# Kernel tuning notes

Hardware: AMD Instinct MI355X
Metric: run time of the kernel (lower is better)

Reference implementation:

```python
import jax, jax.numpy as jnp
import numpy as np

EMBED = 1024
HEADS = 16
HEAD_DIM = EMBED // HEADS


def setup_inputs() -> dict:
    key = jax.random.key(0)
    ks = jax.random.split(key, 9)
    B, S = 2, 2048
    values = jax.random.normal(ks[0], (B, S, EMBED), dtype=jnp.float32)
    keys_in = jax.random.normal(ks[1], (B, S, EMBED), dtype=jnp.float32)
    query = jax.random.normal(ks[2], (B, S, EMBED), dtype=jnp.float32)
    mask = jax.random.randint(ks[3], (B, 1, 1, S), 0, 2, dtype=jnp.int32)
    # torch Linear weights: [out_features, in_features], y = x @ W.T
    sc = 1.0 / np.sqrt(HEAD_DIM)
    Wv = jax.random.uniform(ks[4], (HEAD_DIM, HEAD_DIM), jnp.float32, -sc, sc)
    Wk = jax.random.uniform(ks[5], (HEAD_DIM, HEAD_DIM), jnp.float32, -sc, sc)
    Wq = jax.random.uniform(ks[6], (HEAD_DIM, HEAD_DIM), jnp.float32, -sc, sc)
    so = 1.0 / np.sqrt(EMBED)
    Wo = jax.random.uniform(ks[7], (EMBED, EMBED), jnp.float32, -so, so)
    bo = jax.random.uniform(ks[8], (EMBED,), jnp.float32, -so, so)
    return {"values": values, "keys": keys_in, "query": query, "mask": mask,
            "Wv": Wv, "Wk": Wk, "Wq": Wq, "Wo": Wo, "bo": bo}


def reference(values, keys, query, mask, Wv, Wk, Wq, Wo, bo):
    B = query.shape[0]
    # split heads: [B, S, H, D]
    v = values.reshape(B, -1, HEADS, HEAD_DIM)
    k = keys.reshape(B, -1, HEADS, HEAD_DIM)
    q = query.reshape(B, -1, HEADS, HEAD_DIM)
    # per-head shared linear projections (nn.Linear on last dim, no bias)
    v = jnp.einsum('bshd,ed->bshe', v, Wv)
    k = jnp.einsum('bshd,ed->bshe', k, Wk)
    q = jnp.einsum('bshd,ed->bshe', q, Wq)
    # energy: [B, H, Q, K]
    energy = jnp.einsum('bqhd,bkhd->bhqk', q, k)
    energy = jnp.where(mask == 0, jnp.float32(-1e20), energy)
    attn = jax.nn.softmax(energy / jnp.sqrt(jnp.float32(EMBED)), axis=3)
    out = jnp.einsum('bhqk,bkhd->bqhd', attn, v).reshape(B, -1, EMBED)
    return out @ Wo.T + bo
```

## Files before the change

### kernel.cpp

```cpp
#include <hip/hip_runtime.h>
#include <hip/hip_bf16.h>


typedef __attribute__((ext_vector_type(8))) short bf16x8;
typedef __attribute__((ext_vector_type(4))) float f32x4;
typedef __attribute__((ext_vector_type(16))) float f32x16;
typedef __attribute__((ext_vector_type(2))) int i32x2;

__device__ int g_srcidx[2 * 2048];
__device__ int g_NK[2];

__device__ __forceinline__ short f2bf(float x) {
  union { float f; unsigned u; } v; v.f = x;
  unsigned r = v.u + 0x7FFFu + ((v.u >> 16) & 1u);
  return (short)(r >> 16);
}

__device__ __forceinline__ int pack2(float lo, float hi) {
  __hip_bfloat162 h = __float22bfloat162_rn(make_float2(lo, hi));
  int r; __builtin_memcpy(&r, &h, 4); return r;
}

__device__ __forceinline__ bf16x8 cvt8(float4 a, float4 b) {
  bf16x8 r;
  r[0] = f2bf(a.x); r[1] = f2bf(a.y); r[2] = f2bf(a.z); r[3] = f2bf(a.w);
  r[4] = f2bf(b.x); r[5] = f2bf(b.y); r[6] = f2bf(b.z); r[7] = f2bf(b.w);
  return r;
}

__device__ __forceinline__ void plsw(int& a, int& b) {
  i32x2 r = __builtin_amdgcn_permlane32_swap(a, b, false, false);
  a = r[0]; b = r[1];
}
__device__ __forceinline__ float pl_comb_add(float v) {
  int a = __float_as_int(v), b = a;
  i32x2 r = __builtin_amdgcn_permlane32_swap(a, b, false, false);
  return __int_as_float(r[0]) + __int_as_float(r[1]);
}

__device__ __forceinline__ void gll16(const short* g, short* l) {
  __builtin_amdgcn_global_load_lds(
      (const __attribute__((address_space(1))) void*)g,
      (__attribute__((address_space(3))) void*)l, 16, 0, 0);
}

__global__ __launch_bounds__(256) void prep_kernel(
    const int* __restrict__ mask, const float* __restrict__ Wo,
    short* __restrict__ WoB) {
  __shared__ int cnt[256];
  const int t = threadIdx.x;
  if (blockIdx.x < 2) {
    const int b = blockIdx.x;
    const int* m = mask + b * 2048;
    int* sidx = g_srcidx + b * 2048;
    const int base = t * 8;
    int vals[8], lc = 0;
#pragma unroll
    for (int i = 0; i < 8; i++) { vals[i] = (m[base + i] != 0); lc += vals[i]; }
    cnt[t] = lc;
    __syncthreads();
    for (int off = 1; off < 256; off <<= 1) {
      int v = (t >= off) ? cnt[t - off] : 0;
      __syncthreads();
      cnt[t] += v;
      __syncthreads();
    }
    int pos = cnt[t] - lc;
    const int total = cnt[255];
#pragma unroll
    for (int i = 0; i < 8; i++)
      if (vals[i]) sidx[pos++] = base + i;
    for (int j = total + t; j < 2048; j += 256) sidx[j] = 0;
    if (t == 0) g_NK[b] = total;
  } else {
    int i = ((blockIdx.x - 2) * 256 + t) * 8;
    float4 a = *(const float4*)(Wo + i), b2 = *(const float4*)(Wo + i + 4);
    *(bf16x8*)(WoB + i) = cvt8(a, b2);
  }
}

__global__ __launch_bounds__(256) void proj_kernel(
    const float* __restrict__ keys, const float* __restrict__ query,
    const float* __restrict__ values,
    const float* __restrict__ Wk, const float* __restrict__ Wq,
    const float* __restrict__ Wv,
    short* __restrict__ Kp, short* __restrict__ Qp, short* __restrict__ Vt) {
  const int bid0 = blockIdx.x;
  const int t = threadIdx.x;
  const int w = t >> 6, l = t & 63, l15 = l & 15, l4 = l >> 4;
  __shared__ short Al[64 * 64];
  __shared__ short Bl[64 * 64];
  __shared__ short Tl[64 * 66];

  if (bid0 < 2048) {
    int bid = bid0;
    const float* X = keys; const float* W = Wk; short* O = Kp;
    bool isq = false;
    if (bid >= 1024) { X = query; W = Wq; O = Qp; bid -= 1024; isq = true; }
    const int r0 = bid << 6;
    const int bb = r0 >> 15;
    if (!isq) {
      const int j0 = (r0 >> 4) & 2047;
      const int jlim = (g_NK[bb] + 63) & ~63;
      if (j0 >= jlim) return;
    }
#pragma unroll
    for (int i = 0; i < 2; i++) {
      int c = t + (i << 8);
      int row = c >> 3, col8 = c & 7;
      int pc = col8 ^ (row & 7);
      int ri = r0 + row;
      int j = (ri >> 4) & 2047, hh = ri & 15;
      int s = isq ? j : g_srcidx[(bb << 11) + j];
      const float* xs = X + ((size_t)((bb * 2048 + s) * 16 + hh)) * 64 + col8 * 8;
      float4 a0 = *(const float4*)xs, a1 = *(const float4*)(xs + 4);
      *(bf16x8*)&Al[row * 64 + pc * 8] = cvt8(a0, a1);
      const float* wsrc = W + row * 64 + col8 * 8;
      float4 b0 = *(const float4*)wsrc, b1 = *(const float4*)(wsrc + 4);
      *(bf16x8*)&Bl[row * 64 + pc * 8] = cvt8(b0, b1);
    }
    __syncthreads();
    f32x4 acc[4];
#pragma unroll
    for (int i = 0; i < 4; i++) acc[i] = (f32x4){0.f, 0.f, 0.f, 0.f};
#pragma unroll
    for (int kc = 0; kc < 2; kc++) {
      int ar = w * 16 + l15;
      bf16x8 af = *(const bf16x8*)((const char*)Al +
          ((ar * 128 + kc * 64 + l4 * 16) ^ ((ar & 7) << 4)));
#pragma unroll
      for (int ng = 0; ng < 4; ng++) {
        int br = ng * 16 + l15;
        bf16x8 bfr = *(const bf16x8*)((const char*)Bl +
            ((br * 128 + kc * 64 + l4 * 16) ^ ((br & 7) << 4)));
        acc[ng] = __builtin_amdgcn_mfma_f32_16x16x32_bf16(af, bfr, acc[ng], 0, 0, 0);
      }
    }
    const float osc = isq ? (1.4426950408889634f / 32.0f) : 1.0f;
#pragma unroll
    for (int ng = 0; ng < 4; ng++) {
#pragma unroll
      for (int j = 0; j < 4; j++) {
        int ri = r0 + w * 16 + l4 * 4 + j;
        int e = ng * 16 + l15;
        int b2 = ri >> 15, jj = (ri >> 4) & 2047, hh = ri & 15;
        O[(((size_t)(b2 * 16 + hh)) * 2048 + jj) * 64 + e] = f2bf(acc[ng][j] * osc);
      }
    }
  } else {
    const int bid = bid0 - 2048;
    const int st = bid & 31, bh = bid >> 5;
    const int b = bh >> 4, h = bh & 15;
    const int s0 = st << 6;
    const int jlim = (g_NK[b] + 63) & ~63;
    if (s0 >= jlim) return;
#pragma unroll
    for (int i = 0; i < 2; i++) {
      int c = t + (i << 8);
      int row = c >> 3, col8 = c & 7;
      int pc = col8 ^ (row & 7);
      int s = g_srcidx[(b << 11) + s0 + row];
      const float* xs = values + ((size_t)(b * 2048 + s)) * 1024 + h * 64 + col8 * 8;
      float4 a0 = *(const float4*)xs, a1 = *(const float4*)(xs + 4);
      *(bf16x8*)&Al[row * 64 + pc * 8] = cvt8(a0, a1);
      const float* wsrc = Wv + row * 64 + col8 * 8;
      float4 b0 = *(const float4*)wsrc, b1 = *(const float4*)(wsrc + 4);
      *(bf16x8*)&Bl[row * 64 + pc * 8] = cvt8(b0, b1);
    }
    __syncthreads();
    f32x4 acc[4];
#pragma unroll
    for (int i = 0; i < 4; i++) acc[i] = (f32x4){0.f, 0.f, 0.f, 0.f};
#pragma unroll
    for (int kc = 0; kc < 2; kc++) {
      int ar = w * 16 + l15;
      bf16x8 af = *(const bf16x8*)((const char*)Al +
          ((ar * 128 + kc * 64 + l4 * 16) ^ ((ar & 7) << 4)));
#pragma unroll
      for (int ng = 0; ng < 4; ng++) {
        int br = ng * 16 + l15;
        bf16x8 bfr = *(const bf16x8*)((const char*)Bl +
            ((br * 128 + kc * 64 + l4 * 16) ^ ((br & 7) << 4)));
        acc[ng] = __builtin_amdgcn_mfma_f32_16x16x32_bf16(af, bfr, acc[ng], 0, 0, 0);
      }
    }
#pragma unroll
    for (int ng = 0; ng < 4; ng++) {
#pragma unroll
      for (int j = 0; j < 4; j++) {
        Tl[(w * 16 + l4 * 4 + j) * 66 + ng * 16 + l15] = f2bf(acc[ng][j]);
      }
    }
    __syncthreads();
    int e = t >> 2, sc = (t & 3) << 4;
    bf16x8 o0, o1;
#pragma unroll
    for (int i = 0; i < 8; i++) {
      o0[i] = Tl[(sc + i) * 66 + e];
      o1[i] = Tl[(sc + 8 + i) * 66 + e];
    }
    short* dst = Vt + ((size_t)bh * 64 + e) * 2048 + s0 + sc;
    *(bf16x8*)dst = o0;
    *(bf16x8*)(dst + 8) = o1;
  }
}

__global__ __launch_bounds__(256, 2) void attn_kernel(
    const short* __restrict__ Qp, const short* __restrict__ Kp,
    const short* __restrict__ Vt, short* __restrict__ AO) {
  const int bid = blockIdx.x;
  const int qb = bid & 15, bh = bid >> 4;
  const int b = bh >> 4, h = bh & 15;
  const int t = threadIdx.x;
  const int w = t >> 6, l = t & 63, l31 = l & 31, hi = l >> 5;
  const int q0w = qb * 128 + w * 32;

  __shared__ short Kl[2][64 * 64];
  __shared__ short Vl[2][64 * 64];
  __shared__ float Cl[4 * 32];

  const short* Kbase = Kp + (size_t)bh * 2048 * 64;
  const short* Vbase = Vt + (size_t)bh * 64 * 2048;

  const int nk = g_NK[b];
  const int ntiles = (nk + 63) >> 6;

  const short* qptr = Qp + ((size_t)bh * 2048 + q0w + l31) * 64 + hi * 8;
  bf16x8 qf[4];
#pragma unroll
  for (int dc = 0; dc < 4; dc++) qf[dc] = *(const bf16x8*)(qptr + dc * 16);

  int laddr[2][4];
#pragma unroll
  for (int x = 0; x < 2; x++) {
    int rr = x * 32 + l31;
#pragma unroll
    for (int c2 = 0; c2 < 4; c2++)
      laddr[x][c2] = rr * 128 + (((c2 * 32) + hi * 16) ^ ((rr & 7) << 4));
  }

  const int srow = t >> 3, scol = t & 7;
  const int sc0 = (scol ^ (srow & 7)) * 8;
  const short* ksrc0 = Kbase + srow * 64 + sc0;
  const short* ksrc1 = Kbase + (srow + 32) * 64 + sc0;
  const short* vsrc0 = Vbase + (size_t)srow * 2048 + sc0;
  const short* vsrc1 = Vbase + (size_t)(srow + 32) * 2048 + sc0;
  short* klds = &Kl[0][0];
  short* vlds = &Vl[0][0];
  const int d0 = t * 8, d1 = t * 8 + 2048;

  gll16(ksrc0, klds + d0);
  gll16(ksrc1, klds + d1);
  gll16(vsrc0, vlds + d0);
  gll16(vsrc1, vlds + d1);
  __syncthreads();

  float l_run = 0.f;
  f32x16 o0, o1;
#pragma unroll
  for (int r = 0; r < 16; r++) { o0[r] = 0.f; o1[r] = 0.f; }

  for (int kt = 0; kt < ntiles; kt++) {
    const int bs = kt & 1;
    const int bsb = bs << 13;
    if (kt + 1 < ntiles) {
      const int nb = (bs ^ 1) << 12;
      gll16(ksrc0 + (kt + 1) * 4096, klds + nb + d0);
      gll16(ksrc1 + (kt + 1) * 4096, klds + nb + d1);
      gll16(vsrc0 + (kt + 1) * 64, vlds + nb + d0);
      gll16(vsrc1 + (kt + 1) * 64, vlds + nb + d1);
    }

    f32x16 st0, st1;
#pragma unroll
    for (int r = 0; r < 16; r++) { st0[r] = 0.f; st1[r] = 0.f; }
    __builtin_amdgcn_s_setprio(1);
#pragma unroll
    for (int dc = 0; dc < 4; dc++) {
      bf16x8 ka = *(const bf16x8*)((const char*)Kl + bsb + laddr[0][dc]);
      st0 = __builtin_amdgcn_mfma_f32_32x32x16_bf16(ka, qf[dc], st0, 0, 0, 0);
    }
#pragma unroll
    for (int dc = 0; dc < 4; dc++) {
      bf16x8 kb = *(const bf16x8*)((const char*)Kl + bsb + laddr[1][dc]);
      st1 = __builtin_amdgcn_mfma_f32_32x32x16_bf16(kb, qf[dc], st1, 0, 0, 0);
    }
    __builtin_amdgcn_s_setprio(0);

    if (((kt << 6) + 64) <= nk) {
#pragma unroll
      for (int r = 0; r < 16; r++) {
        st0[r] = __builtin_amdgcn_exp2f(st0[r]);
        st1[r] = __builtin_amdgcn_exp2f(st1[r]);
      }
    } else {
      const int kb2 = kt << 6;
#pragma unroll
      for (int r = 0; r < 16; r++) {
        int cr = (r & 3) + 8 * (r >> 2) + 4 * hi;
        float e0 = __builtin_amdgcn_exp2f(st0[r]);
        float e1 = __builtin_amdgcn_exp2f(st1[r]);
        st0[r] = (kb2 + cr < nk) ? e0 : 0.f;
        st1[r] = (kb2 + 32 + cr < nk) ? e1 : 0.f;
      }
    }

    float sx[8];
#pragma unroll
    for (int i = 0; i < 8; i++)
      sx[i] = (st0[2 * i] + st0[2 * i + 1]) + (st1[2 * i] + st1[2 * i + 1]);
#pragma unroll
    for (int s2 = 4; s2 > 0; s2 >>= 1)
#pragma unroll
      for (int i = 0; i < 4; i++)
        if (i < s2) sx[i] += sx[i + s2];
    l_run += pl_comb_add(sx[0]);

    bf16x8 pa[4];
#pragma unroll
    for (int kc = 0; kc < 4; kc++) {
      int bse = (kc & 1) * 8;
      float p0, p1, p2, p3, p4, p5, p6, p7;
      if (kc < 2) {
        p0 = st0[bse + 0]; p1 = st0[bse + 1]; p2 = st0[bse + 2]; p3 = st0[bse + 3];
        p4 = st0[bse + 4]; p5 = st0[bse + 5]; p6 = st0[bse + 6]; p7 = st0[bse + 7];
      } else {
        p0 = st1[bse + 0]; p1 = st1[bse + 1]; p2 = st1[bse + 2]; p3 = st1[bse + 3];
        p4 = st1[bse + 4]; p5 = st1[bse + 5]; p6 = st1[bse + 6]; p7 = st1[bse + 7];
      }
      int A0 = pack2(p0, p1), A1 = pack2(p2, p3);
      int B0 = pack2(p4, p5), B1 = pack2(p6, p7);
      plsw(A0, B0);
      plsw(A1, B1);
      union { int4 i; bf16x8 h; } u;
      u.i = make_int4(A0, A1, B0, B1);
      pa[kc] = u.h;
    }

    __builtin_amdgcn_s_setprio(1);
#pragma unroll
    for (int kc = 0; kc < 4; kc++) {
      bf16x8 vf = *(const bf16x8*)((const char*)Vl + bsb + laddr[0][kc]);
      o0 = __builtin_amdgcn_mfma_f32_32x32x16_bf16(pa[kc], vf, o0, 0, 0, 0);
    }
#pragma unroll
    for (int kc = 0; kc < 4; kc++) {
      bf16x8 vf = *(const bf16x8*)((const char*)Vl + bsb + laddr[1][kc]);
      o1 = __builtin_amdgcn_mfma_f32_32x32x16_bf16(pa[kc], vf, o1, 0, 0, 0);
    }
    __builtin_amdgcn_s_setprio(0);
    __syncthreads();
  }

  float invr = 1.0f / l_run;
  Cl[w * 32 + l31] = invr;
  short* aob = AO + ((size_t)(b * 2048 + q0w)) * 1024 + h * 64 + l31;
#pragma unroll
  for (int r = 0; r < 16; r++) {
    int qr = (r & 3) + 8 * (r >> 2) + 4 * hi;
    float ic = Cl[w * 32 + qr];
    aob[(size_t)qr * 1024] = f2bf(o0[r] * ic);
    aob[(size_t)qr * 1024 + 32] = f2bf(o1[r] * ic);
  }
}

__global__ __launch_bounds__(256) void outproj_kernel(
    const short* __restrict__ AO, const short* __restrict__ WoB,
    const float* __restrict__ bo, float* __restrict__ Cout) {
  const int bid = blockIdx.x;
  const int mt = bid >> 4, nt = bid & 15;
  const int m0 = mt << 6, n0 = nt << 6;
  const int t = threadIdx.x;
  const int w = t >> 6, l = t & 63, l15 = l & 15, l4 = l >> 4;
  __shared__ short Al[2][64 * 64];
  __shared__ short Bl[2][64 * 64];

  const int srow = t >> 3, scol = t & 7;
  const int sc0 = (scol ^ (srow & 7)) * 8;
  const short* asrc0 = AO + (size_t)(m0 + srow) * 1024 + sc0;
  const short* asrc1 = AO + (size_t)(m0 + srow + 32) * 1024 + sc0;
  const short* bsrc0 = WoB + (size_t)(n0 + srow) * 1024 + sc0;
  const short* bsrc1 = WoB + (size_t)(n0 + srow + 32) * 1024 + sc0;
  short* al = &Al[0][0];
  short* bl = &Bl[0][0];
  const int d0 = t * 8, d1 = t * 8 + 2048;

  gll16(asrc0, al + d0); gll16(asrc1, al + d1);
  gll16(bsrc0, bl + d0); gll16(bsrc1, bl + d1);
  __syncthreads();

  f32x4 acc[4];
#pragma unroll
  for (int i = 0; i < 4; i++) acc[i] = (f32x4){0.f, 0.f, 0.f, 0.f};

  for (int ks = 0; ks < 16; ks++) {
    const int bs = ks & 1, bsb = bs << 13;
    if (ks < 15) {
      const int nb = (bs ^ 1) << 12;
      const int ko = (ks + 1) * 64;
      gll16(asrc0 + ko, al + nb + d0); gll16(asrc1 + ko, al + nb + d1);
      gll16(bsrc0 + ko, bl + nb + d0); gll16(bsrc1 + ko, bl + nb + d1);
    }
#pragma unroll
    for (int kc = 0; kc < 2; kc++) {
      int ar = w * 16 + l15;
      bf16x8 af = *(const bf16x8*)((const char*)Al + bsb +
          ((ar * 128 + kc * 64 + l4 * 16) ^ ((ar & 7) << 4)));
#pragma unroll
      for (int ng = 0; ng < 4; ng++) {
        int br = ng * 16 + l15;
        bf16x8 bfr = *(const bf16x8*)((const char*)Bl + bsb +
            ((br * 128 + kc * 64 + l4 * 16) ^ ((br & 7) << 4)));
        acc[ng] = __builtin_amdgcn_mfma_f32_16x16x32_bf16(af, bfr, acc[ng], 0, 0, 0);
      }
    }
    __syncthreads();
  }
#pragma unroll
  for (int ng = 0; ng < 4; ng++) {
    int n = n0 + ng * 16 + l15;
    float bias = bo[n];
#pragma unroll
    for (int j = 0; j < 4; j++) {
      int m = m0 + w * 16 + l4 * 4 + j;
      Cout[(size_t)m * 1024 + n] = acc[ng][j] + bias;
    }
  }
}

extern "C" void kernel_launch(void* const* d_in, const int* in_sizes, int n_in,
                              void* d_out, int out_size, void* d_ws, size_t ws_size,
                              hipStream_t stream) {
  const float* values = (const float*)d_in[0];
  const float* keys   = (const float*)d_in[1];
  const float* query  = (const float*)d_in[2];
  const int*   mask   = (const int*)d_in[3];
  const float* Wv = (const float*)d_in[4];
  const float* Wk = (const float*)d_in[5];
  const float* Wq = (const float*)d_in[6];
  const float* Wo = (const float*)d_in[7];
  const float* bo = (const float*)d_in[8];
  float* out = (float*)d_out;
  char* ws = (char*)d_ws;
  short* Qp  = (short*)(ws + (size_t)0);
  short* Kp  = (short*)(ws + ((size_t)8 << 20));
  short* Vtp = (short*)(ws + ((size_t)16 << 20));
  short* AO  = (short*)(ws + ((size_t)24 << 20));
  short* WoB = (short*)(ws + ((size_t)32 << 20));

  prep_kernel<<<514, 256, 0, stream>>>(mask, Wo, WoB);
  proj_kernel<<<3072, 256, 0, stream>>>(keys, query, values, Wk, Wq, Wv, Kp, Qp, Vtp);
  attn_kernel<<<512, 256, 0, stream>>>(Qp, Kp, Vtp, AO);
  outproj_kernel<<<1024, 256, 0, stream>>>(AO, WoB, bo, out);
}
```

Before: 70.03 us.

## Process two K/V tiles per barrier with four-buffer LDS pipelining

Restructures the attention main loop so that two 64-key tiles are staged ahead and computed per iteration, with four LDS buffers for K and V. Only one __syncthreads is needed per two tiles, which halves the barrier count, and loads run further ahead of use. It also rewrites cvt8 to use packed bf16 conversions. The cost is doubled LDS use (64KB+ per block), which could lower occupancy below the two blocks per CU the launch bounds request.

After: 70.57 us. Within noise of the previous version (+0.8%).

```diff
diff --git a/kernel.cpp b/kernel.cpp
--- a/kernel.cpp
+++ b/kernel.cpp
@@ -22,10 +22,12 @@
 }
 
 __device__ __forceinline__ bf16x8 cvt8(float4 a, float4 b) {
-  bf16x8 r;
-  r[0] = f2bf(a.x); r[1] = f2bf(a.y); r[2] = f2bf(a.z); r[3] = f2bf(a.w);
-  r[4] = f2bf(b.x); r[5] = f2bf(b.y); r[6] = f2bf(b.z); r[7] = f2bf(b.w);
-  return r;
+  union { int i[4]; bf16x8 h; } u;
+  u.i[0] = pack2(a.x, a.y);
+  u.i[1] = pack2(a.z, a.w);
+  u.i[2] = pack2(b.x, b.y);
+  u.i[3] = pack2(b.z, b.w);
+  return u.h;
 }
 
 __device__ __forceinline__ void plsw(int& a, int& b) {
@@ -215,8 +217,8 @@
   const int w = t >> 6, l = t & 63, l31 = l & 31, hi = l >> 5;
   const int q0w = qb * 128 + w * 32;
 
-  __shared__ short Kl[2][64 * 64];
-  __shared__ short Vl[2][64 * 64];
+  __shared__ short Kl[4][64 * 64];
+  __shared__ short Vl[4][64 * 64];
   __shared__ float Cl[4 * 32];
 
   const short* Kbase = Kp + (size_t)bh * 2048 * 64;
@@ -249,28 +251,21 @@
   short* vlds = &Vl[0][0];
   const int d0 = t * 8, d1 = t * 8 + 2048;
 
-  gll16(ksrc0, klds + d0);
-  gll16(ksrc1, klds + d1);
-  gll16(vsrc0, vlds + d0);
-  gll16(vsrc1, vlds + d1);
-  __syncthreads();
-
   float l_run = 0.f;
   f32x16 o0, o1;
 #pragma unroll
   for (int r = 0; r < 16; r++) { o0[r] = 0.f; o1[r] = 0.f; }
 
-  for (int kt = 0; kt < ntiles; kt++) {
-    const int bs = kt & 1;
-    const int bsb = bs << 13;
-    if (kt + 1 < ntiles) {
-      const int nb = (bs ^ 1) << 12;
-      gll16(ksrc0 + (kt + 1) * 4096, klds + nb + d0);
-      gll16(ksrc1 + (kt + 1) * 4096, klds + nb + d1);
-      gll16(vsrc0 + (kt + 1) * 64, vlds + nb + d0);
-      gll16(vsrc1 + (kt + 1) * 64, vlds + nb + d1);
-    }
-
+  auto stage = [&](int kt, int bufi) {
+    const int off = bufi << 12;
+    gll16(ksrc0 + kt * 4096, klds + off + d0);
+    gll16(ksrc1 + kt * 4096, klds + off + d1);
+    gll16(vsrc0 + kt * 64, vlds + off + d0);
+    gll16(vsrc1 + kt * 64, vlds + off + d1);
+  };
+
+  auto compute = [&](int kt, int bufi) {
+    const int bsb = bufi << 13;
     f32x16 st0, st1;
 #pragma unroll
     for (int r = 0; r < 16; r++) { st0[r] = 0.f; st1[r] = 0.f; }
@@ -349,6 +344,20 @@
       o1 = __builtin_amdgcn_mfma_f32_32x32x16_bf16(pa[kc], vf, o1, 0, 0, 0);
     }
     __builtin_amdgcn_s_setprio(0);
+  };
+
+  stage(0, 0);
+  if (ntiles > 1) stage(1, 1);
+  __syncthreads();
+
+  for (int kt = 0; kt < ntiles; kt += 2) {
+    const int p = (kt >> 1) & 1;
+    const int cb = p * 2;
+    const int nb = (1 - p) * 2;
+    if (kt + 2 < ntiles) stage(kt + 2, nb);
+    if (kt + 3 < ntiles) stage(kt + 3, nb + 1);
+    compute(kt, cb);
+    if (kt + 1 < ntiles) compute(kt + 1, cb + 1);
     __syncthreads();
   }
 
```
